# Kernel optimization log

Measured on AMD Instinct MI355X. Metric: run time of the kernel, lower is better.

The kernel has to match this reference:

```python
import jax, jax.numpy as jnp
import numpy as np
from functools import partial

INPUT_DIM = 22
HIDDEN = 64
LAYERS = 3
OUT = 4
B, T = 1024, 512


def _lstm_layer(x_seq, w_ih, w_hh, b_ih, b_hh):
    # x_seq: [B, T, Din]; gate order (PyTorch): i, f, g, o
    Bsz = x_seq.shape[0]
    H = w_hh.shape[1]
    # precompute input projections for all timesteps: [B, T, 4H]
    x_proj = jnp.einsum('bti,gi->btg', x_seq, w_ih) + b_ih + b_hh

    def step(carry, xp):
        h, c = carry
        gates = xp + h @ w_hh.T  # [B, 4H]
        i, f, g, o = jnp.split(gates, 4, axis=-1)
        i = jax.nn.sigmoid(i)
        f = jax.nn.sigmoid(f)
        g = jnp.tanh(g)
        o = jax.nn.sigmoid(o)
        c = f * c + i * g
        h = o * jnp.tanh(c)
        return (h, c), h

    init = (jnp.zeros((Bsz, H), x_seq.dtype), jnp.zeros((Bsz, H), x_seq.dtype))
    _, hs = jax.lax.scan(step, init, jnp.swapaxes(x_proj, 0, 1))  # [T, B, H]
    return jnp.swapaxes(hs, 0, 1)  # [B, T, H]


def setup_inputs() -> dict:
    key = jax.random.key(0)
    ks = jax.random.split(key, 16)
    inp = {'x': jax.random.normal(ks[0], (B, INPUT_DIM, T), dtype=jnp.float32)}
    k = 1.0 / np.sqrt(HIDDEN)
    i = 1
    for l in range(LAYERS):
        din = INPUT_DIM if l == 0 else HIDDEN
        inp[f'w_ih{l}'] = jax.random.uniform(ks[i], (4 * HIDDEN, din), minval=-k, maxval=k); i += 1
        inp[f'w_hh{l}'] = jax.random.uniform(ks[i], (4 * HIDDEN, HIDDEN), minval=-k, maxval=k); i += 1
        inp[f'b_ih{l}'] = jax.random.uniform(ks[i], (4 * HIDDEN,), minval=-k, maxval=k); i += 1
        inp[f'b_hh{l}'] = jax.random.uniform(ks[i], (4 * HIDDEN,), minval=-k, maxval=k); i += 1
    inp['w_fc'] = jax.random.uniform(ks[i], (OUT, HIDDEN), minval=-k, maxval=k); i += 1
    inp['b_fc'] = jax.random.uniform(ks[i], (OUT,), minval=-k, maxval=k)
    return inp


def reference(x, w_ih0, w_hh0, b_ih0, b_hh0, w_ih1, w_hh1, b_ih1, b_hh1,
              w_ih2, w_hh2, b_ih2, b_hh2, w_fc, b_fc):
    # x: [B, 22, T] -> batch_first [B, T, 22]
    h = jnp.transpose(x, (0, 2, 1))
    h = _lstm_layer(h, w_ih0, w_hh0, b_ih0, b_hh0)
    # inter-layer dropout(0.4) is identity in eval/inference mode
    h = _lstm_layer(h, w_ih1, w_hh1, b_ih1, b_hh1)
    h = _lstm_layer(h, w_ih2, w_hh2, b_ih2, b_hh2)
    last = h[:, -1, :]  # [B, H]
    return last @ w_fc.T + b_fc  # [B, 4]
```

## Files before the change

kernel.cpp:

```cpp
#include <hip/hip_runtime.h>


#define TT   512
#define NTH  768
#define NBLK 256

typedef _Float16 h16;
typedef __attribute__((ext_vector_type(8))) _Float16 h16x8;
typedef __attribute__((ext_vector_type(4))) float f32x4;

#define MFMA16(a, b, c) __builtin_amdgcn_mfma_f32_16x16x32_f16((a), (b), (c), 0, 0, 0)

#define NLOG2E  -1.4426950408889634f
#define N2LOG2E -2.8853900817779268f

__device__ __forceinline__ h16x8 loadB(const float* __restrict__ W, int ld, int ro,
                                       int k0, int kmax, float scale) {
    h16x8 r;
    #pragma unroll
    for (int i = 0; i < 8; ++i) {
        const int k = k0 + i;
        r[i] = (h16)((k < kmax) ? scale * W[(size_t)ro * ld + k] : 0.f);
    }
    return r;
}

struct TrueC  { static constexpr bool value = true;  };
struct FalseC { static constexpr bool value = false; };

__global__ __attribute__((amdgpu_flat_work_group_size(NTH, NTH), amdgpu_waves_per_eu(3)))
void lstm_mfma(
    const float* __restrict__ x,
    const float* __restrict__ wih0, const float* __restrict__ whh0,
    const float* __restrict__ bih0, const float* __restrict__ bhh0,
    const float* __restrict__ wih1, const float* __restrict__ whh1,
    const float* __restrict__ bih1, const float* __restrict__ bhh1,
    const float* __restrict__ wih2, const float* __restrict__ whh2,
    const float* __restrict__ bih2, const float* __restrict__ bhh2,
    const float* __restrict__ wfc, const float* __restrict__ bfc,
    float* __restrict__ out)
{
    const int tid  = threadIdx.x;
    const int w    = tid >> 6;
    const int wl   = w >> 2;
    const int wg   = w & 3;
    const int lane = tid & 63;
    const int nloc = lane & 15;
    const int kg   = lane >> 4;
    const int b4   = blockIdx.x * 4;
    const int u    = wg * 16 + nloc;

    __shared__ alignas(16) h16 XL[2 * 32 * 512];
    __shared__ alignas(16) h16 HT[3 * 2 * 1024];
    __shared__ h16 PAD[3072];

    h16x8 Bf[4][4];
    float bias[4];
    #pragma unroll
    for (int g = 0; g < 4; ++g) {
        const int ro = g * 64 + u;
        const float sc = (g == 2) ? N2LOG2E : NLOG2E;
        if (wl == 0) {
            Bf[g][0] = loadB(wih0, 22, ro, kg * 8,      22, sc);
            Bf[g][1] = loadB(whh0, 64, ro, kg * 8,      64, sc);
            Bf[g][2] = loadB(whh0, 64, ro, 32 + kg * 8, 64, sc);
            Bf[g][3] = Bf[g][2];
            bias[g]  = sc * (bih0[ro] + bhh0[ro]);
        } else if (wl == 1) {
            Bf[g][0] = loadB(wih1, 64, ro, kg * 8,      64, sc);
            Bf[g][1] = loadB(wih1, 64, ro, 32 + kg * 8, 64, sc);
            Bf[g][2] = loadB(whh1, 64, ro, kg * 8,      64, sc);
            Bf[g][3] = loadB(whh1, 64, ro, 32 + kg * 8, 64, sc);
            bias[g]  = sc * (bih1[ro] + bhh1[ro]);
        } else {
            Bf[g][0] = loadB(wih2, 64, ro, kg * 8,      64, sc);
            Bf[g][1] = loadB(wih2, 64, ro, 32 + kg * 8, 64, sc);
            Bf[g][2] = loadB(whh2, 64, ro, kg * 8,      64, sc);
            Bf[g][3] = loadB(whh2, 64, ro, 32 + kg * 8, 64, sc);
            bias[g]  = sc * (bih2[ro] + bhh2[ro]);
        }
    }

    if (bias[0] > 1.0e30f) { PAD[tid & 2047] = (h16)bias[0]; out[0] = (float)PAD[0]; }

    {
        int* xz = (int*)XL;
        for (int i = tid; i < 2 * 32 * 256; i += NTH) xz[i] = 0;
        int* hz = (int*)HT;
        for (int i = tid; i < 3 * 2 * 512; i += NTH) hz[i] = 0;
    }
    __syncthreads();

    auto stage_x = [&](int chunk) {
        if (tid < 4 * 22) {
            const int bl = tid / 22, ii = tid - bl * 22;
            const float* src = x + (size_t)(b4 + bl) * (22 * 512) + (size_t)ii * 512
                                 + chunk * 32;
            h16* dst = &XL[(chunk & 1) * (32 * 512) + (ii >> 3) * 128 + (4 * bl) * 8 + (ii & 7)];
            #pragma unroll
            for (int q = 0; q < 8; ++q) {
                const float4 v = ((const float4*)src)[q];
                dst[(q * 4 + 0) * 512] = (h16)v.x;
                dst[(q * 4 + 1) * 512] = (h16)v.y;
                dst[(q * 4 + 2) * 512] = (h16)v.z;
                dst[(q * 4 + 3) * 512] = (h16)v.w;
            }
        }
    };
    stage_x(0);

    const int lo8  = lane * 8;
    const int hoff = (u >> 3) * 128 + kg * 32 + (u & 7);

    float cst = 0.f;

    auto ew = [&](const f32x4& zi, const f32x4& zf, const f32x4& zg, const f32x4& zo,
                  h16* hb) {
        const float ei = __builtin_amdgcn_exp2f(zi[0]);
        const float ef = __builtin_amdgcn_exp2f(zf[0]);
        const float eg = __builtin_amdgcn_exp2f(zg[0]);
        const float eo = __builtin_amdgcn_exp2f(zo[0]);
        const float pig = (1.f + ei) * (1.f + eg);
        const float pf  = 1.f + ef;
        const float n   = cst * pig + (1.f - eg) * pf;
        const float c   = n * __builtin_amdgcn_rcpf(pf * pig);
        cst = c;
        const float ea  = fminf(c * N2LOG2E, 126.f);
        const float ec  = __builtin_amdgcn_exp2f(ea);
        const float h   = (1.f - ec)
                        * __builtin_amdgcn_rcpf((1.f + ec) * (1.f + eo));
        hb[hoff] = (h16)h;
    };

    f32x4 zb[4];
    #pragma unroll
    for (int g = 0; g < 4; ++g) zb[g] = f32x4{bias[g], 0.f, 0.f, 0.f};

    __syncthreads();

    f32x4 zc[4];
    if (wl == 0) {
        const h16x8 ax0 = *(const h16x8*)&XL[lo8];
        #pragma unroll
        for (int g = 0; g < 4; ++g) zc[g] = MFMA16(ax0, Bf[g][0], zb[g]);
    } else {
        #pragma unroll
        for (int g = 0; g < 4; ++g) zc[g] = zb[g];
    }

    auto tick = [&](int t, auto edgec) {
        constexpr bool EDGE = decltype(edgec)::value;
        const int wb = t & 1, rb = wb ^ 1;
        const h16* h0r = HT + 0 * 2048 + rb * 1024;
        h16*       h0w = HT + 0 * 2048 + wb * 1024;
        const h16* h1r = HT + 1 * 2048 + rb * 1024;
        h16*       h1w = HT + 1 * 2048 + wb * 1024;
        const h16* h2r = HT + 2 * 2048 + rb * 1024;
        h16*       h2w = HT + 2 * 2048 + wb * 1024;

        if (wl == 0) {
            const bool sa = !EDGE || (t < TT);
            const bool ia = !EDGE || (t < TT - 1);
            f32x4 z[4];
            h16x8 a0lo, a0hi, axn;
            if (sa) {
                a0lo = *(const h16x8*)(h0r + lo8);
                a0hi = *(const h16x8*)(h0r + lo8 + 512);
            }
            if (ia) {
                const int tn = t + 1;
                axn = *(const h16x8*)&XL[((tn >> 5) & 1) * (32 * 512) + (tn & 31) * 512 + lo8];
            }
            if (sa) {
                #pragma unroll
                for (int g = 0; g < 4; ++g) {
                    z[g] = MFMA16(a0lo, Bf[g][1], zc[g]);
                    z[g] = MFMA16(a0hi, Bf[g][2], z[g]);
                }
            }
            if ((t & 31) == 16 && (t >> 5) < 15) stage_x((t >> 5) + 1);
            if (sa) ew(z[0], z[1], z[2], z[3], h0w);
            if (ia) {
                #pragma unroll
                for (int g = 0; g < 4; ++g)
                    zc[g] = MFMA16(axn, Bf[g][0], zb[g]);
            }
        } else if (wl == 1) {
            const bool sa = !EDGE || (t >= 2 && t < TT + 2);
            const bool ia = !EDGE || (t >= 1 && t < TT + 1);
            f32x4 z[4];
            h16x8 a1lo, a1hi, a0lo, a0hi;
            if (sa) {
                a1lo = *(const h16x8*)(h1r + lo8);
                a1hi = *(const h16x8*)(h1r + lo8 + 512);
            }
            if (ia) {
                a0lo = *(const h16x8*)(h0r + lo8);
                a0hi = *(const h16x8*)(h0r + lo8 + 512);
            }
            if (sa) {
                #pragma unroll
                for (int g = 0; g < 4; ++g) {
                    z[g] = MFMA16(a1lo, Bf[g][2], zc[g]);
                    z[g] = MFMA16(a1hi, Bf[g][3], z[g]);
                }
            }
            if (sa) ew(z[0], z[1], z[2], z[3], h1w);
            if (ia) {
                #pragma unroll
                for (int g = 0; g < 4; ++g) {
                    f32x4 zn = MFMA16(a0lo, Bf[g][0], zb[g]);
                    zc[g] = MFMA16(a0hi, Bf[g][1], zn);
                }
            }
        } else {
            const bool sa = !EDGE || (t >= 4);
            const bool ia = !EDGE || (t >= 3 && t < TT + 3);
            f32x4 z[4];
            h16x8 a2lo, a2hi, a1lo, a1hi;
            if (sa) {
                a2lo = *(const h16x8*)(h2r + lo8);
                a2hi = *(const h16x8*)(h2r + lo8 + 512);
            }
            if (ia) {
                a1lo = *(const h16x8*)(h1r + lo8);
                a1hi = *(const h16x8*)(h1r + lo8 + 512);
            }
            if (sa) {
                #pragma unroll
                for (int g = 0; g < 4; ++g) {
                    z[g] = MFMA16(a2lo, Bf[g][2], zc[g]);
                    z[g] = MFMA16(a2hi, Bf[g][3], z[g]);
                }
            }
            if (sa) ew(z[0], z[1], z[2], z[3], h2w);
            if (ia) {
                #pragma unroll
                for (int g = 0; g < 4; ++g) {
                    f32x4 zn = MFMA16(a1lo, Bf[g][0], zb[g]);
                    zc[g] = MFMA16(a1hi, Bf[g][1], zn);
                }
            }
        }

        __syncthreads();
    };

    #pragma unroll 1
    for (int t = 0; t < 4; ++t) tick(t, TrueC{});
    #pragma unroll 1
    for (int t = 4; t < TT - 1; ++t) tick(t, FalseC{});
    #pragma unroll 1
    for (int t = TT - 1; t < TT + 4; ++t) tick(t, TrueC{});

    if (tid < 16) {
        const int ms = tid >> 2, o = tid & 3;
        const h16* h2 = HT + 2 * 2048 + 1024;
        float acc = bfc[o];
        #pragma unroll 1
        for (int uu = 0; uu < 64; ++uu)
            acc += (float)h2[(uu >> 3) * 128 + (4 * ms) * 8 + (uu & 7)] * wfc[o * 64 + uu];
        out[(b4 + ms) * 4 + o] = acc;
    }
}

extern "C" void kernel_launch(void* const* d_in, const int* in_sizes, int n_in,
                              void* d_out, int out_size, void* d_ws, size_t ws_size,
                              hipStream_t stream) {
    const float* x    = (const float*)d_in[0];
    const float* wih0 = (const float*)d_in[1];
    const float* whh0 = (const float*)d_in[2];
    const float* bih0 = (const float*)d_in[3];
    const float* bhh0 = (const float*)d_in[4];
    const float* wih1 = (const float*)d_in[5];
    const float* whh1 = (const float*)d_in[6];
    const float* bih1 = (const float*)d_in[7];
    const float* bhh1 = (const float*)d_in[8];
    const float* wih2 = (const float*)d_in[9];
    const float* whh2 = (const float*)d_in[10];
    const float* bih2 = (const float*)d_in[11];
    const float* bhh2 = (const float*)d_in[12];
    const float* wfc  = (const float*)d_in[13];
    const float* bfc  = (const float*)d_in[14];
    float* out = (float*)d_out;

    lstm_mfma<<<dim3(NBLK), dim3(NTH), 0, stream>>>(
        x, wih0, whh0, bih0, bhh0, wih1, whh1, bih1, bhh1,
        wih2, whh2, bih2, bhh2, wfc, bfc, out);
}
```

Baseline: 380.5 us.

## Batch input projections across four timesteps per MFMA with deeper hidden-state ring

Restructures the layer-pipelined LSTM so each layer computes the input projection for four consecutive timesteps in one MFMA. The four timesteps are packed into the batch/column slots that were previously padding, and each result is then split out as the accumulator seed for that step's recurrent update. The hidden-state buffers become an 8-deep ring per layer so that four-step groups can read the previous layer's outputs, and the layer skew is widened to one group (four steps). The intent is to remove most of the per-step input-projection MFMAs from the serial critical path. In exchange it uses more LDS, increases the pipeline fill/drain steps, and drops the old LDS padding array that limited occupancy.

```diff
diff --git a/kernel.cpp b/kernel.cpp
--- a/kernel.cpp
+++ b/kernel.cpp
@@ -51,8 +51,7 @@
     const int u    = wg * 16 + nloc;
 
     __shared__ alignas(16) h16 XL[2 * 32 * 512];
-    __shared__ alignas(16) h16 HT[3 * 2 * 1024];
-    __shared__ h16 PAD[3072];
+    __shared__ alignas(16) h16 HR[3 * 8 * 1024];
 
     h16x8 Bf[4][4];
     float bias[4];
@@ -81,13 +80,11 @@
         }
     }
 
-    if (bias[0] > 1.0e30f) { PAD[tid & 2047] = (h16)bias[0]; out[0] = (float)PAD[0]; }
-
     {
         int* xz = (int*)XL;
         for (int i = tid; i < 2 * 32 * 256; i += NTH) xz[i] = 0;
-        int* hz = (int*)HT;
-        for (int i = tid; i < 3 * 2 * 512; i += NTH) hz[i] = 0;
+        int* hz = (int*)HR;
+        for (int i = tid; i < 3 * 8 * 512; i += NTH) hz[i] = 0;
     }
     __syncthreads();
 
@@ -111,6 +108,8 @@
 
     const int lo8  = lane * 8;
     const int hoff = (u >> 3) * 128 + kg * 32 + (u & 7);
+    const int bj   = lane & 3;
+    const int boff = (lane >> 4) * 128 + ((lane & 15) >> 2) * 32;
 
     float cst = 0.f;
 
@@ -132,130 +131,127 @@
         hb[hoff] = (h16)h;
     };
 
-    f32x4 zb[4];
-    #pragma unroll
-    for (int g = 0; g < 4; ++g) zb[g] = f32x4{bias[g], 0.f, 0.f, 0.f};
-
     __syncthreads();
 
-    f32x4 zc[4];
-    if (wl == 0) {
-        const h16x8 ax0 = *(const h16x8*)&XL[lo8];
-        #pragma unroll
-        for (int g = 0; g < 4; ++g) zc[g] = MFMA16(ax0, Bf[g][0], zb[g]);
-    } else {
-        #pragma unroll
-        for (int g = 0; g < 4; ++g) zc[g] = zb[g];
-    }
-
-    auto tick = [&](int t, auto edgec) {
+    h16* const HR0 = HR;
+    h16* const HR1 = HR + 8192;
+    h16* const HR2 = HR + 16384;
+
+    auto group = [&](int G, auto edgec) {
         constexpr bool EDGE = decltype(edgec)::value;
-        const int wb = t & 1, rb = wb ^ 1;
-        const h16* h0r = HT + 0 * 2048 + rb * 1024;
-        h16*       h0w = HT + 0 * 2048 + wb * 1024;
-        const h16* h1r = HT + 1 * 2048 + rb * 1024;
-        h16*       h1w = HT + 1 * 2048 + wb * 1024;
-        const h16* h2r = HT + 2 * 2048 + rb * 1024;
-        h16*       h2w = HT + 2 * 2048 + wb * 1024;
+        f32x4 zB[4];
 
         if (wl == 0) {
-            const bool sa = !EDGE || (t < TT);
-            const bool ia = !EDGE || (t < TT - 1);
-            f32x4 z[4];
-            h16x8 a0lo, a0hi, axn;
-            if (sa) {
-                a0lo = *(const h16x8*)(h0r + lo8);
-                a0hi = *(const h16x8*)(h0r + lo8 + 512);
-            }
-            if (ia) {
-                const int tn = t + 1;
-                axn = *(const h16x8*)&XL[((tn >> 5) & 1) * (32 * 512) + (tn & 31) * 512 + lo8];
-            }
-            if (sa) {
+            const bool act = !EDGE || (G <= 127);
+            if (act) {
+                const int t0 = 4 * G;
+                const h16x8 axB = *(const h16x8*)
+                    &XL[((t0 >> 5) & 1) * 16384 + ((t0 & 31) + bj) * 512 + boff];
                 #pragma unroll
                 for (int g = 0; g < 4; ++g) {
-                    z[g] = MFMA16(a0lo, Bf[g][1], zc[g]);
-                    z[g] = MFMA16(a0hi, Bf[g][2], z[g]);
-                }
-            }
-            if ((t & 31) == 16 && (t >> 5) < 15) stage_x((t >> 5) + 1);
-            if (sa) ew(z[0], z[1], z[2], z[3], h0w);
-            if (ia) {
-                #pragma unroll
-                for (int g = 0; g < 4; ++g)
-                    zc[g] = MFMA16(axn, Bf[g][0], zb[g]);
+                    const f32x4 zb4 = {bias[g], bias[g], bias[g], bias[g]};
+                    zB[g] = MFMA16(axB, Bf[g][0], zb4);
+                }
+            }
+            #pragma unroll
+            for (int j = 0; j < 4; ++j) {
+                if (act) {
+                    const int t = 4 * G + j;
+                    const h16* sr = HR0 + ((t - 1) & 7) * 1024;
+                    h16*       sw = HR0 + (t & 7) * 1024;
+                    const h16x8 alo = *(const h16x8*)(sr + lo8);
+                    const h16x8 ahi = *(const h16x8*)(sr + lo8 + 512);
+                    f32x4 z[4];
+                    #pragma unroll
+                    for (int g = 0; g < 4; ++g) {
+                        const f32x4 cin = {zB[g][j], 0.f, 0.f, 0.f};
+                        z[g] = MFMA16(alo, Bf[g][1], cin);
+                        z[g] = MFMA16(ahi, Bf[g][2], z[g]);
+                    }
+                    if (j == 0 && (G & 7) == 4 && (G >> 3) < 15) stage_x((G >> 3) + 1);
+                    ew(z[0], z[1], z[2], z[3], sw);
+                }
+                __syncthreads();
             }
         } else if (wl == 1) {
-            const bool sa = !EDGE || (t >= 2 && t < TT + 2);
-            const bool ia = !EDGE || (t >= 1 && t < TT + 1);
-            f32x4 z[4];
-            h16x8 a1lo, a1hi, a0lo, a0hi;
-            if (sa) {
-                a1lo = *(const h16x8*)(h1r + lo8);
-                a1hi = *(const h16x8*)(h1r + lo8 + 512);
-            }
-            if (ia) {
-                a0lo = *(const h16x8*)(h0r + lo8);
-                a0hi = *(const h16x8*)(h0r + lo8 + 512);
-            }
-            if (sa) {
+            const bool act = !EDGE || (G >= 1 && G <= 128);
+            if (act) {
+                const int sB = 4 * G - 4;
+                const h16* hb = HR0 + ((sB + bj) & 7) * 1024 + boff;
+                const h16x8 blo = *(const h16x8*)hb;
+                const h16x8 bhi = *(const h16x8*)(hb + 512);
                 #pragma unroll
                 for (int g = 0; g < 4; ++g) {
-                    z[g] = MFMA16(a1lo, Bf[g][2], zc[g]);
-                    z[g] = MFMA16(a1hi, Bf[g][3], z[g]);
-                }
-            }
-            if (sa) ew(z[0], z[1], z[2], z[3], h1w);
-            if (ia) {
+                    const f32x4 zb4 = {bias[g], bias[g], bias[g], bias[g]};
+                    f32x4 zt = MFMA16(blo, Bf[g][0], zb4);
+                    zB[g] = MFMA16(bhi, Bf[g][1], zt);
+                }
+            }
+            #pragma unroll
+            for (int j = 0; j < 4; ++j) {
+                if (act) {
+                    const int s = 4 * G - 4 + j;
+                    const h16* sr = HR1 + ((s - 1) & 7) * 1024;
+                    h16*       sw = HR1 + (s & 7) * 1024;
+                    const h16x8 alo = *(const h16x8*)(sr + lo8);
+                    const h16x8 ahi = *(const h16x8*)(sr + lo8 + 512);
+                    f32x4 z[4];
+                    #pragma unroll
+                    for (int g = 0; g < 4; ++g) {
+                        const f32x4 cin = {zB[g][j], 0.f, 0.f, 0.f};
+                        z[g] = MFMA16(alo, Bf[g][2], cin);
+                        z[g] = MFMA16(ahi, Bf[g][3], z[g]);
+                    }
+                    ew(z[0], z[1], z[2], z[3], sw);
+                }
+                __syncthreads();
+            }
+        } else {
+            const bool act = !EDGE || (G >= 2);
+            if (act) {
+                const int sB = 4 * G - 8;
+                const h16* hb = HR1 + ((sB + bj) & 7) * 1024 + boff;
+                const h16x8 blo = *(const h16x8*)hb;
+                const h16x8 bhi = *(const h16x8*)(hb + 512);
                 #pragma unroll
                 for (int g = 0; g < 4; ++g) {
-                    f32x4 zn = MFMA16(a0lo, Bf[g][0], zb[g]);
-                    zc[g] = MFMA16(a0hi, Bf[g][1], zn);
-                }
-            }
-        } else {
-            const bool sa = !EDGE || (t >= 4);
-            const bool ia = !EDGE || (t >= 3 && t < TT + 3);
-            f32x4 z[4];
-            h16x8 a2lo, a2hi, a1lo, a1hi;
-            if (sa) {
-                a2lo = *(const h16x8*)(h2r + lo8);
-                a2hi = *(const h16x8*)(h2r + lo8 + 512);
-            }
-            if (ia) {
-                a1lo = *(const h16x8*)(h1r + lo8);
-                a1hi = *(const h16x8*)(h1r + lo8 + 512);
-            }
-            if (sa) {
-                #pragma unroll
-                for (int g = 0; g < 4; ++g) {
-                    z[g] = MFMA16(a2lo, Bf[g][2], zc[g]);
-                    z[g] = MFMA16(a2hi, Bf[g][3], z[g]);
-                }
-            }
-            if (sa) ew(z[0], z[1], z[2], z[3], h2w);
-            if (ia) {
-                #pragma unroll
-                for (int g = 0; g < 4; ++g) {
-                    f32x4 zn = MFMA16(a1lo, Bf[g][0], zb[g]);
-                    zc[g] = MFMA16(a1hi, Bf[g][1], zn);
-                }
+                    const f32x4 zb4 = {bias[g], bias[g], bias[g], bias[g]};
+                    f32x4 zt = MFMA16(blo, Bf[g][0], zb4);
+                    zB[g] = MFMA16(bhi, Bf[g][1], zt);
+                }
+            }
+            #pragma unroll
+            for (int j = 0; j < 4; ++j) {
+                if (act) {
+                    const int s = 4 * G - 8 + j;
+                    const h16* sr = HR2 + ((s - 1) & 7) * 1024;
+                    h16*       sw = HR2 + (s & 7) * 1024;
+                    const h16x8 alo = *(const h16x8*)(sr + lo8);
+                    const h16x8 ahi = *(const h16x8*)(sr + lo8 + 512);
+                    f32x4 z[4];
+                    #pragma unroll
+                    for (int g = 0; g < 4; ++g) {
+                        const f32x4 cin = {zB[g][j], 0.f, 0.f, 0.f};
+                        z[g] = MFMA16(alo, Bf[g][2], cin);
+                        z[g] = MFMA16(ahi, Bf[g][3], z[g]);
+                    }
+                    ew(z[0], z[1], z[2], z[3], sw);
+                }
+                __syncthreads();
             }
         }
-
-        __syncthreads();
     };
 
+    group(0, TrueC{});
+    group(1, TrueC{});
     #pragma unroll 1
-    for (int t = 0; t < 4; ++t) tick(t, TrueC{});
-    #pragma unroll 1
-    for (int t = 4; t < TT - 1; ++t) tick(t, FalseC{});
-    #pragma unroll 1
-    for (int t = TT - 1; t < TT + 4; ++t) tick(t, TrueC{});
+    for (int G = 2; G < 128; ++G) group(G, FalseC{});
+    group(128, TrueC{});
+    group(129, TrueC{});
 
     if (tid < 16) {
         const int ms = tid >> 2, o = tid & 3;
-        const h16* h2 = HT + 2 * 2048 + 1024;
+        const h16* h2 = HR2 + 7 * 1024;
         float acc = bfc[o];
         #pragma unroll 1
         for (int uu = 0; uu < 64; ++uu)
```

After: 351.8 us. -7.5%, faster.
